# Kernel tuning notes

Hardware: AMD Instinct MI355X
Metric: run time of the kernel (lower is better)

The kernel has to match this reference:

```python
import jax, jax.numpy as jnp
import numpy as np

K = 3       # kernel_size
STRIDE = 1
PAD = 1


def conv3d(x, w, b):
    # standard Conv3d NCDHW, used to predict per-tap offsets
    y = jax.lax.conv_general_dilated(
        x, w, window_strides=(STRIDE,) * 3, padding=[(PAD, PAD)] * 3,
        dimension_numbers=("NCDHW", "OIDHW", "NCDHW"))
    return y + b[None, :, None, None, None]


def trilinear_sample(xn, pd, ph, pw):
    # xn: (C,D,H,W); pd/ph/pw: (T,Do,Ho,Wo) float voxel coords.
    # Trilinear interpolation with zeros padding (grid_sample semantics).
    C, D, H, W = xn.shape
    d0 = jnp.floor(pd); h0 = jnp.floor(ph); w0 = jnp.floor(pw)
    fd = pd - d0; fh = ph - h0; fw = pw - w0
    d0 = d0.astype(jnp.int32); h0 = h0.astype(jnp.int32); w0 = w0.astype(jnp.int32)
    out = jnp.zeros((C,) + pd.shape, xn.dtype)
    for dd in (0, 1):
        wd = fd if dd else 1.0 - fd
        di = d0 + dd
        for hh in (0, 1):
            wh = fh if hh else 1.0 - fh
            hi = h0 + hh
            for ww in (0, 1):
                wc = fw if ww else 1.0 - fw
                wi = w0 + ww
                valid = (di >= 0) & (di < D) & (hi >= 0) & (hi < H) & (wi >= 0) & (wi < W)
                wgt = jnp.where(valid, wd * wh * wc, 0.0)
                g = xn[:, jnp.clip(di, 0, D - 1), jnp.clip(hi, 0, H - 1), jnp.clip(wi, 0, W - 1)]
                out = out + wgt[None] * g
    return out  # (C,T,Do,Ho,Wo)


def deform_conv3d(x, offset, weight):
    # x: (N,C,D,H,W); offset: (N,3*K^3,Do,Ho,Wo); weight: (O,C,K,K,K)
    N, C, D, H, W = x.shape
    Do = (D + 2 * PAD - K) // STRIDE + 1
    Ho = (H + 2 * PAD - K) // STRIDE + 1
    Wo = (W + 2 * PAD - K) // STRIDE + 1
    T = K ** 3
    kd, kh, kw = jnp.meshgrid(jnp.arange(K), jnp.arange(K), jnp.arange(K), indexing="ij")
    kd = kd.reshape(T, 1, 1, 1).astype(x.dtype)
    kh = kh.reshape(T, 1, 1, 1).astype(x.dtype)
    kw = kw.reshape(T, 1, 1, 1).astype(x.dtype)
    base_d = kd - PAD + (jnp.arange(Do, dtype=x.dtype) * STRIDE).reshape(1, Do, 1, 1)
    base_h = kh - PAD + (jnp.arange(Ho, dtype=x.dtype) * STRIDE).reshape(1, 1, Ho, 1)
    base_w = kw - PAD + (jnp.arange(Wo, dtype=x.dtype) * STRIDE).reshape(1, 1, 1, Wo)
    off = offset.reshape(N, 3, T, Do, Ho, Wo)  # matches offset.view(N,3,K,K,K,...) tap ordering
    pd = base_d[None] + off[:, 0]
    ph = base_h[None] + off[:, 1]
    pw = base_w[None] + off[:, 2]
    sampled = jax.vmap(trilinear_sample)(x, pd, ph, pw)  # (N,C,T,Do,Ho,Wo)
    O = weight.shape[0]
    w2 = weight.reshape(O, C, T)
    return jnp.einsum("nctdhw,oct->nodhw", sampled, w2)


def setup_inputs() -> dict:
    key = jax.random.key(0)
    k1, k2, k3 = jax.random.split(key, 3)
    N, C, O, S = 2, 16, 32, 48
    x = jax.random.normal(k1, (N, C, S, S, S), jnp.float32)
    fan_in = C * K ** 3
    weight = jax.random.normal(k2, (O, C, K, K, K), jnp.float32) * (1.0 / np.sqrt(fan_in))
    # offset conv params; small scale so sampled positions stay near the base grid
    offset_w = jax.random.normal(k3, (3 * K ** 3, C, K, K, K), jnp.float32) * 0.02
    offset_b = jnp.zeros((3 * K ** 3,), jnp.float32)
    return {"x": x, "weight": weight, "offset_w": offset_w, "offset_b": offset_b}


def reference(x, weight, offset_w, offset_b):
    offset = conv3d(x, offset_w, offset_b)
    return deform_conv3d(x, offset, weight)
```

## Files before the change

kernel.cpp:

```cpp
#include <hip/hip_runtime.h>
#include <hip/hip_fp16.h>

#define SDIM 48
#define SP   110592
#define C_IN 16
#define O_OUT 32
#define T27  27
#define OST  96
#define OLROW 100
#define CPST 36

typedef __attribute__((ext_vector_type(8))) _Float16 f16x8;
typedef __attribute__((ext_vector_type(4))) float f32x4;

__device__ __forceinline__ float h2f(unsigned short u) {
    return __half2float(__builtin_bit_cast(__half, u));
}
__device__ __forceinline__ unsigned short f2h(float f) {
    __half h = __float2half(f);
    return __builtin_bit_cast(unsigned short, h);
}

__global__ __launch_bounds__(256)
void prep_xT(const float* __restrict__ x, unsigned short* __restrict__ xT) {
    __shared__ float l[256 * 17];
    const int tid = threadIdx.x;
    const int b   = blockIdx.x;
    const int n   = b / 432;
    const int sp0 = (b - n * 432) * 256;
    #pragma unroll
    for (int c = 0; c < 16; ++c)
        l[tid * 17 + c] = x[((size_t)(n * 16 + c)) * SP + sp0 + tid];
    __syncthreads();
    unsigned int u[8];
    #pragma unroll
    for (int q = 0; q < 8; ++q) {
        unsigned short a  = f2h(l[tid * 17 + 2 * q]);
        unsigned short bb = f2h(l[tid * 17 + 2 * q + 1]);
        u[q] = (unsigned int)a | ((unsigned int)bb << 16);
    }
    uint4* dst = (uint4*)(xT + ((size_t)(n * SP + sp0 + tid)) * 16);
    dst[0] = make_uint4(u[0], u[1], u[2], u[3]);
    dst[1] = make_uint4(u[4], u[5], u[6], u[7]);
}

__global__ __launch_bounds__(256)
void prep_bfrag(const float* __restrict__ ow, unsigned short* __restrict__ Bf) {
    int idx = blockIdx.x * 256 + threadIdx.x;
    int r    = idx & 7;
    int lane = (idx >> 3) & 63;
    int snt  = idx >> 9;
    int s = snt / 6, nt = snt - s * 6;
    int kk  = ((lane >> 4) << 3) + r;
    int g   = nt * 16 + (lane & 15);
    int tap = 2 * s + (kk >> 4);
    int c   = kk & 15;
    float v = 0.f;
    if (tap < 27 && g < 81) v = ow[((size_t)(g * 16 + c)) * 27 + tap];
    Bf[idx] = f2h(v);
}

__global__ __launch_bounds__(256)
void prep_wfrag(const float* __restrict__ w, unsigned short* __restrict__ Wf) {
    int idx = blockIdx.x * 256 + threadIdx.x;
    int r    = idx & 7;
    int lane = (idx >> 3) & 63;
    int snt  = idx >> 9;
    int s = snt >> 1, nt = snt & 1;
    int kk  = ((lane >> 4) << 3) + r;
    int o   = nt * 16 + (lane & 15);
    int tap = 2 * s + (kk >> 4);
    int c   = kk & 15;
    float v = 0.f;
    if (tap < 27) v = w[((size_t)(o * 16 + c)) * 27 + tap];
    Wf[idx] = f2h(v);
}

__global__ __launch_bounds__(256)
void offs_conv_mfma(const unsigned short* __restrict__ xT,
                    const unsigned short* __restrict__ Bf,
                    const float* __restrict__ ob,
                    unsigned short* __restrict__ offs) {
    __shared__ unsigned short Alds[256 * 8];
    __shared__ unsigned short Tl[64 * 104];
    const int tid  = threadIdx.x;
    const int lane = tid & 63;
    const int wid  = tid >> 6;
    const int bid  = (blockIdx.x & 7) * 432 + (blockIdx.x >> 3);
    const int m    = tid & 63;
    const int n    = (bid >= 1728) ? 1 : 0;
    const int sp   = bid * 64 + m - n * SP;
    const int z    = sp / 2304;
    const int rem  = sp - z * 2304;
    const int y    = rem / 48;
    const int xx   = rem - y * 48;
    const int tapoff = wid >> 1;
    const int half   = wid & 1;

    auto stage_load = [&](int s) -> uint4 {
        int tap = 2 * s + tapoff;
        int kd = tap / 9;
        int t2 = tap - kd * 9;
        int kh = t2 / 3;
        int kw = t2 - kh * 3;
        int di = z + kd - 1, hi = y + kh - 1, wi = xx + kw - 1;
        bool ok = (tap < 27) && ((unsigned)di < 48u) && ((unsigned)hi < 48u) &&
                  ((unsigned)wi < 48u);
        uint4 v = make_uint4(0u, 0u, 0u, 0u);
        if (ok) {
            size_t off = ((size_t)(n * SP + (di * 2304 + hi * 48 + wi))) * 16 + half * 8;
            v = *(const uint4*)(xT + off);
        }
        return v;
    };

    f32x4 acc[6];
    #pragma unroll
    for (int t = 0; t < 6; ++t) acc[t] = (f32x4){0.f, 0.f, 0.f, 0.f};

    uint4 v = stage_load(0);
    for (int s = 0; s < 14; ++s) {
        __syncthreads();
        *(uint4*)&Alds[tid * 8] = v;
        __syncthreads();
        if (s < 13) v = stage_load(s + 1);
        f16x8 a = *(const f16x8*)&Alds[(((lane >> 4) * 64) + (wid * 16) + (lane & 15)) * 8];
        const f16x8* bp = (const f16x8*)Bf + (size_t)(s * 6) * 64 + lane;
        #pragma unroll
        for (int nt = 0; nt < 6; ++nt) {
            f16x8 b = bp[nt * 64];
            acc[nt] = __builtin_amdgcn_mfma_f32_16x16x32_f16(a, b, acc[nt], 0, 0, 0);
        }
    }

    const int mrow = wid * 16 + ((lane >> 4) << 2);
    #pragma unroll
    for (int nt = 0; nt < 6; ++nt) {
        int g = nt * 16 + (lane & 15);
        float bia = (g < 81) ? ob[g] : 0.f;
        #pragma unroll
        for (int r = 0; r < 4; ++r)
            Tl[(mrow + r) * 104 + g] = f2h(acc[nt][r] + bia);
    }
    __syncthreads();
    unsigned short* dst = offs + (size_t)bid * (64 * OST);
    #pragma unroll
    for (int k = 0; k < 3; ++k) {
        int idx = k * 256 + tid;
        int row = idx / 12;
        int col = (idx - row * 12) * 8;
        uint4 vv = *(const uint4*)&Tl[row * 104 + col];
        *(uint4*)(dst + row * OST + col) = vv;
    }
}

__global__ __launch_bounds__(448, 4)
void deform_fused(const unsigned short* __restrict__ xT,
                  const unsigned short* __restrict__ Wf,
                  const unsigned short* __restrict__ offs,
                  float* __restrict__ out) {
    __shared__ unsigned short OLDS[32 * OLROW];
    __shared__ float Cp[7 * 32 * CPST];

    const int tid  = threadIdx.x;
    const int lane = tid & 63;
    const int wv   = tid >> 6;
    const int pl   = lane & 15;
    const int chh  = (lane >> 4) & 1;
    const int tl   = lane >> 5;
    const int bid  = (blockIdx.x & 7) * 864 + (blockIdx.x >> 3);
    const int n    = (bid >= 3456) ? 1 : 0;
    const int sp0  = bid * 32 - n * SP;

    if (tid < 384) {
        int row = tid / 12;
        int col = (tid - row * 12) * 8;
        uint4 v = *(const uint4*)(offs + ((size_t)(n * SP + sp0 + row)) * OST + col);
        *(uint4*)&OLDS[row * OLROW + col] = v;
    }
    __syncthreads();

    const uint4* xq4 = (const uint4*)(xT + (size_t)n * SP * 16);

    f32x4 acc[2][2];
    #pragma unroll
    for (int a_ = 0; a_ < 2; ++a_)
        #pragma unroll
        for (int b_ = 0; b_ < 2; ++b_) acc[a_][b_] = (f32x4){0.f, 0.f, 0.f, 0.f};

    #pragma unroll
    for (int pg = 0; pg < 2; ++pg) {
        const int p  = pg * 16 + pl;
        const int sp = sp0 + p;
        const int z  = sp / 2304;
        const int rm = sp - z * 2304;
        const int y  = rm / 48;
        const int xx = rm - y * 48;

        #pragma unroll
        for (int s2 = 0; s2 < 2; ++s2) {
            const int s   = 2 * wv + s2;
            const int tap = 2 * s + tl;
            uint4 au = make_uint4(0u, 0u, 0u, 0u);
            if (tap < 27) {
                const int kd = tap / 9;
                const int t2 = tap - kd * 9;
                const int kh = t2 / 3;
                const int kw = t2 - kh * 3;
                float pd = (float)(z + kd - 1)  + h2f(OLDS[p * OLROW + tap]);
                float ph = (float)(y + kh - 1)  + h2f(OLDS[p * OLROW + 27 + tap]);
                float pw = (float)(xx + kw - 1) + h2f(OLDS[p * OLROW + 54 + tap]);
                float df = floorf(pd), hf = floorf(ph), wf = floorf(pw);
                float fd = pd - df, fh = ph - hf, fw = pw - wf;
                int d0 = (int)df, h0 = (int)hf, w0 = (int)wf;
                float wd0 = ((unsigned)d0       < 48u) ? (1.f - fd) : 0.f;
                float wd1 = ((unsigned)(d0 + 1) < 48u) ? fd : 0.f;
                float wh0 = ((unsigned)h0       < 48u) ? (1.f - fh) : 0.f;
                float wh1 = ((unsigned)(h0 + 1) < 48u) ? fh : 0.f;
                float ww0 = ((unsigned)w0       < 48u) ? (1.f - fw) : 0.f;
                float ww1 = ((unsigned)(w0 + 1) < 48u) ? fw : 0.f;
                int dc0 = min(max(d0,     0), 47) * 2304;
                int dc1 = min(max(d0 + 1, 0), 47) * 2304;
                int hc0 = min(max(h0,     0), 47) * 48;
                int hc1 = min(max(h0 + 1, 0), 47) * 48;
                int wc0 = min(max(w0,     0), 47);
                int wc1 = min(max(w0 + 1, 0), 47);

                float wdh[4] = {wd0 * wh0, wd0 * wh1, wd1 * wh0, wd1 * wh1};
                int   rdh[4] = {dc0 + hc0, dc0 + hc1, dc1 + hc0, dc1 + hc1};

                uint4 cv[8];
                float cw[8];
                #pragma unroll
                for (int jj = 0; jj < 8; ++jj) {
                    int dh = jj >> 1;
                    int ws = jj & 1;
                    int idx = rdh[dh] + (ws ? wc1 : wc0);
                    cv[jj] = xq4[(size_t)idx * 2 + chh];
                    cw[jj] = wdh[dh] * (ws ? ww1 : ww0);
                }

                float sm[8];
                #pragma unroll
                for (int q = 0; q < 8; ++q) sm[q] = 0.f;
                #pragma unroll
                for (int jj = 0; jj < 8; ++jj) {
                    float w_ = cw[jj];
                    unsigned int uu[4] = {cv[jj].x, cv[jj].y, cv[jj].z, cv[jj].w};
                    #pragma unroll
                    for (int q = 0; q < 4; ++q) {
                        asm("v_fma_mix_f32 %0, %1, %2, %0 op_sel:[0,0,0] op_sel_hi:[1,0,0]"
                            : "+v"(sm[2 * q]) : "v"(uu[q]), "v"(w_));
                        asm("v_fma_mix_f32 %0, %1, %2, %0 op_sel:[1,0,0] op_sel_hi:[1,0,0]"
                            : "+v"(sm[2 * q + 1]) : "v"(uu[q]), "v"(w_));
                    }
                }
                unsigned int o0, o1, o2, o3;
                asm("v_cvt_pkrtz_f16_f32 %0, %1, %2" : "=v"(o0) : "v"(sm[0]), "v"(sm[1]));
                asm("v_cvt_pkrtz_f16_f32 %0, %1, %2" : "=v"(o1) : "v"(sm[2]), "v"(sm[3]));
                asm("v_cvt_pkrtz_f16_f32 %0, %1, %2" : "=v"(o2) : "v"(sm[4]), "v"(sm[5]));
                asm("v_cvt_pkrtz_f16_f32 %0, %1, %2" : "=v"(o3) : "v"(sm[6]), "v"(sm[7]));
                au = make_uint4(o0, o1, o2, o3);
            }
            f16x8 a = __builtin_bit_cast(f16x8, au);
            const f16x8* bp = (const f16x8*)Wf + (size_t)(s * 2) * 64 + lane;
            acc[pg][0] = __builtin_amdgcn_mfma_f32_16x16x32_f16(a, bp[0],  acc[pg][0], 0, 0, 0);
            acc[pg][1] = __builtin_amdgcn_mfma_f32_16x16x32_f16(a, bp[64], acc[pg][1], 0, 0, 0);
        }
    }

    {
        const int o16 = lane & 15;
        const int m0  = (lane >> 4) << 2;
        #pragma unroll
        for (int pg = 0; pg < 2; ++pg) {
            *(f32x4*)&Cp[(wv * 32 + o16)      * CPST + pg * 16 + m0] = acc[pg][0];
            *(f32x4*)&Cp[(wv * 32 + 16 + o16) * CPST + pg * 16 + m0] = acc[pg][1];
        }
    }
    __syncthreads();

    #pragma unroll
    for (int rep = 0; rep < 3; ++rep) {
        int i = tid + rep * 448;
        if (i < 1024) {
            int o = i >> 5;
            int m = i & 31;
            float r0 = 0.f;
            #pragma unroll
            for (int w2 = 0; w2 < 7; ++w2)
                r0 += Cp[(w2 * 32 + o) * CPST + m];
            out[((size_t)(n * O_OUT + o)) * SP + sp0 + m] = r0;
        }
    }
}

extern "C" void kernel_launch(void* const* d_in, const int* in_sizes, int n_in,
                              void* d_out, int out_size, void* d_ws, size_t ws_size,
                              hipStream_t stream) {
    (void)in_sizes; (void)n_in; (void)out_size; (void)ws_size;
    const float* x      = (const float*)d_in[0];
    const float* weight = (const float*)d_in[1];
    const float* ow     = (const float*)d_in[2];
    const float* ob     = (const float*)d_in[3];
    float* out = (float*)d_out;

    unsigned short* offs_b = (unsigned short*)d_ws;
    unsigned short* xT     = offs_b + (size_t)2 * SP * OST;
    unsigned short* Bf     = xT + (size_t)2 * SP * 16;
    unsigned short* Wf     = Bf + 43008;

    prep_xT<<<864, 256, 0, stream>>>(x, xT);
    prep_bfrag<<<168, 256, 0, stream>>>(ow, Bf);
    prep_wfrag<<<56, 256, 0, stream>>>(weight, Wf);
    offs_conv_mfma<<<3456, 256, 0, stream>>>(xT, Bf, ob, offs_b);
    deform_fused<<<6912, 448, 0, stream>>>(xT, Wf, offs_b, out);
}
```

Baseline: 157.0 us.

## Give each wave its own 16 points across all taps, dropping the LDS reduction

```diff
diff --git a/kernel.cpp b/kernel.cpp
--- a/kernel.cpp
+++ b/kernel.cpp
@@ -8,7 +8,6 @@
 #define T27  27
 #define OST  96
 #define OLROW 100
-#define CPST 36
 
 typedef __attribute__((ext_vector_type(8))) _Float16 f16x8;
 typedef __attribute__((ext_vector_type(4))) float f32x4;
@@ -154,13 +153,12 @@
     }
 }
 
-__global__ __launch_bounds__(448, 4)
+__global__ __launch_bounds__(512, 4)
 void deform_fused(const unsigned short* __restrict__ xT,
                   const unsigned short* __restrict__ Wf,
                   const unsigned short* __restrict__ offs,
                   float* __restrict__ out) {
-    __shared__ unsigned short OLDS[32 * OLROW];
-    __shared__ float Cp[7 * 32 * CPST];
+    __shared__ unsigned short OLDS[128 * OLROW];
 
     const int tid  = threadIdx.x;
     const int lane = tid & 63;
@@ -168,13 +166,15 @@
     const int pl   = lane & 15;
     const int chh  = (lane >> 4) & 1;
     const int tl   = lane >> 5;
-    const int bid  = (blockIdx.x & 7) * 864 + (blockIdx.x >> 3);
-    const int n    = (bid >= 3456) ? 1 : 0;
-    const int sp0  = bid * 32 - n * SP;
-
-    if (tid < 384) {
-        int row = tid / 12;
-        int col = (tid - row * 12) * 8;
+    const int bid  = (blockIdx.x & 7) * 216 + (blockIdx.x >> 3);
+    const int n    = (bid >= 864) ? 1 : 0;
+    const int sp0  = bid * 128 - n * SP;
+
+    #pragma unroll
+    for (int k = 0; k < 3; ++k) {
+        int idx = k * 512 + tid;
+        int row = idx / 12;
+        int col = (idx - row * 12) * 8;
         uint4 v = *(const uint4*)(offs + ((size_t)(n * SP + sp0 + row)) * OST + col);
         *(uint4*)&OLDS[row * OLROW + col] = v;
     }
@@ -182,116 +182,93 @@
 
     const uint4* xq4 = (const uint4*)(xT + (size_t)n * SP * 16);
 
-    f32x4 acc[2][2];
-    #pragma unroll
-    for (int a_ = 0; a_ < 2; ++a_)
-        #pragma unroll
-        for (int b_ = 0; b_ < 2; ++b_) acc[a_][b_] = (f32x4){0.f, 0.f, 0.f, 0.f};
-
-    #pragma unroll
-    for (int pg = 0; pg < 2; ++pg) {
-        const int p  = pg * 16 + pl;
-        const int sp = sp0 + p;
-        const int z  = sp / 2304;
-        const int rm = sp - z * 2304;
-        const int y  = rm / 48;
-        const int xx = rm - y * 48;
-
-        #pragma unroll
-        for (int s2 = 0; s2 < 2; ++s2) {
-            const int s   = 2 * wv + s2;
-            const int tap = 2 * s + tl;
-            uint4 au = make_uint4(0u, 0u, 0u, 0u);
-            if (tap < 27) {
-                const int kd = tap / 9;
-                const int t2 = tap - kd * 9;
-                const int kh = t2 / 3;
-                const int kw = t2 - kh * 3;
-                float pd = (float)(z + kd - 1)  + h2f(OLDS[p * OLROW + tap]);
-                float ph = (float)(y + kh - 1)  + h2f(OLDS[p * OLROW + 27 + tap]);
-                float pw = (float)(xx + kw - 1) + h2f(OLDS[p * OLROW + 54 + tap]);
-                float df = floorf(pd), hf = floorf(ph), wf = floorf(pw);
-                float fd = pd - df, fh = ph - hf, fw = pw - wf;
-                int d0 = (int)df, h0 = (int)hf, w0 = (int)wf;
-                float wd0 = ((unsigned)d0       < 48u) ? (1.f - fd) : 0.f;
-                float wd1 = ((unsigned)(d0 + 1) < 48u) ? fd : 0.f;
-                float wh0 = ((unsigned)h0       < 48u) ? (1.f - fh) : 0.f;
-                float wh1 = ((unsigned)(h0 + 1) < 48u) ? fh : 0.f;
-                float ww0 = ((unsigned)w0       < 48u) ? (1.f - fw) : 0.f;
-                float ww1 = ((unsigned)(w0 + 1) < 48u) ? fw : 0.f;
-                int dc0 = min(max(d0,     0), 47) * 2304;
-                int dc1 = min(max(d0 + 1, 0), 47) * 2304;
-                int hc0 = min(max(h0,     0), 47) * 48;
-                int hc1 = min(max(h0 + 1, 0), 47) * 48;
-                int wc0 = min(max(w0,     0), 47);
-                int wc1 = min(max(w0 + 1, 0), 47);
-
-                float wdh[4] = {wd0 * wh0, wd0 * wh1, wd1 * wh0, wd1 * wh1};
-                int   rdh[4] = {dc0 + hc0, dc0 + hc1, dc1 + hc0, dc1 + hc1};
-
-                uint4 cv[8];
-                float cw[8];
+    const int p  = wv * 16 + pl;
+    const int sp = sp0 + p;
+    const int z  = sp / 2304;
+    const int rm = sp - z * 2304;
+    const int y  = rm / 48;
+    const int xx = rm - y * 48;
+
+    f32x4 acc0 = (f32x4){0.f, 0.f, 0.f, 0.f};
+    f32x4 acc1 = (f32x4){0.f, 0.f, 0.f, 0.f};
+
+    #pragma unroll 2
+    for (int s = 0; s < 14; ++s) {
+        const int tap = 2 * s + tl;
+        uint4 au = make_uint4(0u, 0u, 0u, 0u);
+        if (tap < 27) {
+            const int kd = tap / 9;
+            const int t2 = tap - kd * 9;
+            const int kh = t2 / 3;
+            const int kw = t2 - kh * 3;
+            float pd = (float)(z + kd - 1)  + h2f(OLDS[p * OLROW + tap]);
+            float ph = (float)(y + kh - 1)  + h2f(OLDS[p * OLROW + 27 + tap]);
+            float pw = (float)(xx + kw - 1) + h2f(OLDS[p * OLROW + 54 + tap]);
+            float df = floorf(pd), hf = floorf(ph), wf = floorf(pw);
+            float fd = pd - df, fh = ph - hf, fw = pw - wf;
+            int d0 = (int)df, h0 = (int)hf, w0 = (int)wf;
+            float wd0 = ((unsigned)d0       < 48u) ? (1.f - fd) : 0.f;
+            float wd1 = ((unsigned)(d0 + 1) < 48u) ? fd : 0.f;
+            float wh0 = ((unsigned)h0       < 48u) ? (1.f - fh) : 0.f;
+            float wh1 = ((unsigned)(h0 + 1) < 48u) ? fh : 0.f;
+            float ww0 = ((unsigned)w0       < 48u) ? (1.f - fw) : 0.f;
+            float ww1 = ((unsigned)(w0 + 1) < 48u) ? fw : 0.f;
+            int dc0 = min(max(d0,     0), 47) * 2304;
+            int dc1 = min(max(d0 + 1, 0), 47) * 2304;
+            int hc0 = min(max(h0,     0), 47) * 48;
+            int hc1 = min(max(h0 + 1, 0), 47) * 48;
+            int wc0 = min(max(w0,     0), 47);
+            int wc1 = min(max(w0 + 1, 0), 47);
+
+            float wdh[4] = {wd0 * wh0, wd0 * wh1, wd1 * wh0, wd1 * wh1};
+            int   rdh[4] = {dc0 + hc0, dc0 + hc1, dc1 + hc0, dc1 + hc1};
+
+            uint4 cv[8];
+            float cw[8];
+            #pragma unroll
+            for (int jj = 0; jj < 8; ++jj) {
+                int dh = jj >> 1;
+                int ws = jj & 1;
+                int idx = rdh[dh] + (ws ? wc1 : wc0);
+                cv[jj] = xq4[(size_t)idx * 2 + chh];
+                cw[jj] = wdh[dh] * (ws ? ww1 : ww0);
+            }
+
+            float sm[8];
+            #pragma unroll
+            for (int q = 0; q < 8; ++q) sm[q] = 0.f;
+            #pragma unroll
+            for (int jj = 0; jj < 8; ++jj) {
+                float w_ = cw[jj];
+                unsigned int uu[4] = {cv[jj].x, cv[jj].y, cv[jj].z, cv[jj].w};
                 #pragma unroll
-                for (int jj = 0; jj < 8; ++jj) {
-                    int dh = jj >> 1;
-                    int ws = jj & 1;
-                    int idx = rdh[dh] + (ws ? wc1 : wc0);
-                    cv[jj] = xq4[(size_t)idx * 2 + chh];
-                    cw[jj] = wdh[dh] * (ws ? ww1 : ww0);
+                for (int q = 0; q < 4; ++q) {
+                    asm("v_fma_mix_f32 %0, %1, %2, %0 op_sel:[0,0,0] op_sel_hi:[1,0,0]"
+                        : "+v"(sm[2 * q]) : "v"(uu[q]), "v"(w_));
+                    asm("v_fma_mix_f32 %0, %1, %2, %0 op_sel:[1,0,0] op_sel_hi:[1,0,0]"
+                        : "+v"(sm[2 * q + 1]) : "v"(uu[q]), "v"(w_));
                 }
-
-                float sm[8];
-                #pragma unroll
-                for (int q = 0; q < 8; ++q) sm[q] = 0.f;
-                #pragma unroll
-                for (int jj = 0; jj < 8; ++jj) {
-                    float w_ = cw[jj];
-                    unsigned int uu[4] = {cv[jj].x, cv[jj].y, cv[jj].z, cv[jj].w};
-                    #pragma unroll
-                    for (int q = 0; q < 4; ++q) {
-                        asm("v_fma_mix_f32 %0, %1, %2, %0 op_sel:[0,0,0] op_sel_hi:[1,0,0]"
-                            : "+v"(sm[2 * q]) : "v"(uu[q]), "v"(w_));
-                        asm("v_fma_mix_f32 %0, %1, %2, %0 op_sel:[1,0,0] op_sel_hi:[1,0,0]"
-                            : "+v"(sm[2 * q + 1]) : "v"(uu[q]), "v"(w_));
-                    }
-                }
-                unsigned int o0, o1, o2, o3;
-                asm("v_cvt_pkrtz_f16_f32 %0, %1, %2" : "=v"(o0) : "v"(sm[0]), "v"(sm[1]));
-                asm("v_cvt_pkrtz_f16_f32 %0, %1, %2" : "=v"(o1) : "v"(sm[2]), "v"(sm[3]));
-                asm("v_cvt_pkrtz_f16_f32 %0, %1, %2" : "=v"(o2) : "v"(sm[4]), "v"(sm[5]));
-                asm("v_cvt_pkrtz_f16_f32 %0, %1, %2" : "=v"(o3) : "v"(sm[6]), "v"(sm[7]));
-                au = make_uint4(o0, o1, o2, o3);
             }
-            f16x8 a = __builtin_bit_cast(f16x8, au);
-            const f16x8* bp = (const f16x8*)Wf + (size_t)(s * 2) * 64 + lane;
-            acc[pg][0] = __builtin_amdgcn_mfma_f32_16x16x32_f16(a, bp[0],  acc[pg][0], 0, 0, 0);
-            acc[pg][1] = __builtin_amdgcn_mfma_f32_16x16x32_f16(a, bp[64], acc[pg][1], 0, 0, 0);
+            unsigned int o0, o1, o2, o3;
+            asm("v_cvt_pkrtz_f16_f32 %0, %1, %2" : "=v"(o0) : "v"(sm[0]), "v"(sm[1]));
+            asm("v_cvt_pkrtz_f16_f32 %0, %1, %2" : "=v"(o1) : "v"(sm[2]), "v"(sm[3]));
+            asm("v_cvt_pkrtz_f16_f32 %0, %1, %2" : "=v"(o2) : "v"(sm[4]), "v"(sm[5]));
+            asm("v_cvt_pkrtz_f16_f32 %0, %1, %2" : "=v"(o3) : "v"(sm[6]), "v"(sm[7]));
+            au = make_uint4(o0, o1, o2, o3);
         }
+        f16x8 a = __builtin_bit_cast(f16x8, au);
+        const f16x8* bp = (const f16x8*)Wf + (size_t)(s * 2) * 64 + lane;
+        acc0 = __builtin_amdgcn_mfma_f32_16x16x32_f16(a, bp[0],  acc0, 0, 0, 0);
+        acc1 = __builtin_amdgcn_mfma_f32_16x16x32_f16(a, bp[64], acc1, 0, 0, 0);
     }
 
     {
-        const int o16 = lane & 15;
-        const int m0  = (lane >> 4) << 2;
-        #pragma unroll
-        for (int pg = 0; pg < 2; ++pg) {
-            *(f32x4*)&Cp[(wv * 32 + o16)      * CPST + pg * 16 + m0] = acc[pg][0];
-            *(f32x4*)&Cp[(wv * 32 + 16 + o16) * CPST + pg * 16 + m0] = acc[pg][1];
-        }
-    }
-    __syncthreads();
-
-    #pragma unroll
-    for (int rep = 0; rep < 3; ++rep) {
-        int i = tid + rep * 448;
-        if (i < 1024) {
-            int o = i >> 5;
-            int m = i & 31;
-            float r0 = 0.f;
-            #pragma unroll
-            for (int w2 = 0; w2 < 7; ++w2)
-                r0 += Cp[(w2 * 32 + o) * CPST + m];
-            out[((size_t)(n * O_OUT + o)) * SP + sp0 + m] = r0;
-        }
+        const int o   = lane & 15;
+        const int row = (lane >> 4) << 2;
+        float* op0 = out + ((size_t)(n * O_OUT + o))      * SP + sp0 + wv * 16 + row;
+        float* op1 = out + ((size_t)(n * O_OUT + 16 + o)) * SP + sp0 + wv * 16 + row;
+        *(float4*)op0 = make_float4(acc0[0], acc0[1], acc0[2], acc0[3]);
+        *(float4*)op1 = make_float4(acc1[0], acc1[1], acc1[2], acc1[3]);
     }
 }
 
@@ -314,5 +291,5 @@
     prep_bfrag<<<168, 256, 0, stream>>>(ow, Bf);
     prep_wfrag<<<56, 256, 0, stream>>>(weight, Wf);
     offs_conv_mfma<<<3456, 256, 0, stream>>>(xT, Bf, ob, offs_b);
-    deform_fused<<<6912, 448, 0, stream>>>(xT, Wf, offs_b, out);
-}
+    deform_fused<<<1728, 512, 0, stream>>>(xT, Wf, offs_b, out);
+}
```

Result: slower. 161.0 us (+2.6%).
